# Optimization experiments

Measured on AMD Instinct MI355X. Metric: run time of the kernel, lower is better.

## Reference

```python
import jax, jax.numpy as jnp
import numpy as np

B, N, G = 16, 6000, 512
NUM_PAD_GT = 64  # zero-padded gt rows per image


def _make_boxes(key, shape):
    # sample two corner points and sort so (y1,x1) <= (y2,x2)
    r = jax.random.uniform(key, shape[:-1] + (4,), dtype=jnp.float32)
    lo = jnp.minimum(r[..., :2], r[..., 2:])
    hi = jnp.maximum(r[..., :2], r[..., 2:])
    return jnp.concatenate([lo, hi], axis=-1)


def setup_inputs() -> dict:
    key = jax.random.key(0)
    k1, k2, k3 = jax.random.split(key, 3)
    rois = _make_boxes(k1, (B, N, 4))
    gt_boxes = _make_boxes(k2, (B, G, 4))
    # zero-pad tail gt rows (remove_zero_padding signal)
    gt_boxes = gt_boxes.at[:, G - NUM_PAD_GT:, :].set(0.0)
    # ids in [-2, 18]: <0 crowd, ==0 padding, >0 real classes
    gt_ids = jax.random.randint(k3, (B, G), 0, 21, dtype=jnp.int64) - 2
    gt_ids = jnp.where(jnp.arange(G) >= G - NUM_PAD_GT, 0, gt_ids)
    return {"rois": rois, "gt_ids": gt_ids, "gt_boxes": gt_boxes}


def _pairwise_iou(boxes1, boxes2):
    # boxes1: [B,N,4], boxes2: [B,G,4] in (y1,x1,y2,x2) -> IoU [B,N,G]
    b1 = boxes1[:, :, None, :]  # [B,N,1,4]
    b2 = boxes2[:, None, :, :]  # [B,1,G,4]
    y1 = jnp.maximum(b1[..., 0], b2[..., 0])
    x1 = jnp.maximum(b1[..., 1], b2[..., 1])
    y2 = jnp.minimum(b1[..., 2], b2[..., 2])
    x2 = jnp.minimum(b1[..., 3], b2[..., 3])
    inter = jnp.maximum(y2 - y1, 0.0) * jnp.maximum(x2 - x1, 0.0)
    area1 = (b1[..., 2] - b1[..., 0]) * (b1[..., 3] - b1[..., 1])
    area2 = (b2[..., 2] - b2[..., 0]) * (b2[..., 3] - b2[..., 1])
    union = area1 + area2 - inter
    return inter / (union + 1e-8)


def reference(rois, gt_ids, gt_boxes):
    # remove_zero_padding -> validity masks (jit-friendly: mask instead of gather)
    valid_roi = jnp.sum(jnp.abs(rois), axis=-1) > 0.0      # [B,N]
    valid_gt = jnp.sum(jnp.abs(gt_boxes), axis=-1) > 0.0   # [B,G]
    crowd = valid_gt & (gt_ids < 0)                          # [B,G]
    non_crowd = valid_gt & (gt_ids > 0)                      # [B,G]

    iou = _pairwise_iou(rois, gt_boxes)                      # [B,N,G]
    # max IoU against non-crowd / crowd gt subsets (masked cols -> 0, IoU >= 0)
    iou_nc_max = jnp.max(jnp.where(non_crowd[:, None, :], iou, 0.0), axis=2)
    iou_c_max = jnp.max(jnp.where(crowd[:, None, :], iou, 0.0), axis=2)
    iou_nc_max = jnp.where(valid_roi, iou_nc_max, 0.0)       # [B,N]
    iou_c_max = jnp.where(valid_roi, iou_c_max, 0.0)

    positive_mask = valid_roi & (iou_nc_max >= 0.5)
    negative_mask = valid_roi & (iou_nc_max < 0.5) & (iou_c_max < 1e-3)

    iou_maxes = jnp.stack([iou_nc_max, iou_c_max], axis=1)   # [B,2,N]
    return iou_maxes, positive_mask, negative_mask
```

## Files before the change

kernel.cpp:

```cpp
#include <hip/hip_runtime.h>

#define BB 16
#define NN 6000
#define GG 512
#define WAVES 8
#define ROIS_PER_BLOCK 128

__global__ __launch_bounds__(64 * WAVES) void det_kernel(
    const float4* __restrict__ rois,
    const int*    __restrict__ gt_ids,
    const float4* __restrict__ gt_boxes,
    float*        __restrict__ out)
{
    __shared__ float4 s_box[GG];
    __shared__ float4 s_area4[GG / 4];
    __shared__ float  s_ncm[WAVES][ROIS_PER_BLOCK];
    __shared__ float  s_cm[WAVES][ROIS_PER_BLOCK];
    __shared__ int    s_cnt[2];
    __shared__ int    s_bounds[2];
    float* s_area = (float*)s_area4;

    const int b    = blockIdx.y;
    const int tid  = threadIdx.x;
    const int wave = tid >> 6;
    const int lane = tid & 63;

    if (tid == 0) { s_cnt[0] = 0; s_cnt[1] = 0; }
    __syncthreads();

    {
        const int g = tid;
        float4 box = gt_boxes[b * GG + g];
        float asum = fabsf(box.x) + fabsf(box.y) + fabsf(box.z) + fabsf(box.w);
        int id = gt_ids[b * GG + g];
        const bool pn = (asum > 0.0f) && (id > 0);
        const bool pc = (asum > 0.0f) && (id < 0);
        unsigned long long mn = __ballot(pn);
        unsigned long long mc = __ballot(pc);
        int bn = 0, bc = 0;
        if (lane == 0) {
            bn = atomicAdd(&s_cnt[0], __popcll(mn));
            bc = atomicAdd(&s_cnt[1], __popcll(mc));
        }
        bn = __shfl(bn, 0);
        bc = __shfl(bc, 0);
        const unsigned long long lt = (1ULL << lane) - 1ULL;
        if (pn) {
            int idx = bn + __popcll(mn & lt);
            s_box[idx]  = box;
            s_area[idx] = (box.z - box.x) * (box.w - box.y);
        }
        if (pc) {
            int idx = (GG - 1) - (bc + __popcll(mc & lt));
            s_box[idx]  = box;
            s_area[idx] = (box.z - box.x) * (box.w - box.y);
        }
    }
    __syncthreads();

    if (tid == 0) {
        int ncnt = s_cnt[0];
        int lo   = GG - s_cnt[1];
        int nc_eff = (ncnt + 3) & ~3;
        int lo_pad = lo & ~3;
        if (nc_eff > lo_pad) nc_eff = lo_pad;
        s_bounds[0] = nc_eff;
        s_bounds[1] = lo_pad;
    }
    __syncthreads();

    const int nc_eff = s_bounds[0];
    const int lo_pad = s_bounds[1];

    {
        const float4 z = make_float4(0.f, 0.f, 0.f, 0.f);
        const int ncnt = s_cnt[0];
        const int lo   = GG - s_cnt[1];
        if (tid < 4) {
            int i = ncnt + tid;
            if (i < nc_eff) { s_box[i] = z; s_area[i] = 0.f; }
        } else if (tid < 8) {
            int i = lo_pad + (tid - 4);
            if (i < lo) { s_box[i] = z; s_area[i] = 0.f; }
        }
    }
    __syncthreads();

    const int nbase = blockIdx.x * ROIS_PER_BLOCK;
    const int n0 = nbase + lane;
    const int n1 = nbase + 64 + lane;
    const float4 z4 = make_float4(0.f, 0.f, 0.f, 0.f);
    const float4 r0 = (n0 < NN) ? rois[b * NN + n0] : z4;
    const float4 r1 = (n1 < NN) ? rois[b * NN + n1] : z4;
    const bool  v0 = (fabsf(r0.x) + fabsf(r0.y) + fabsf(r0.z) + fabsf(r0.w)) > 0.0f;
    const bool  v1 = (fabsf(r1.x) + fabsf(r1.y) + fabsf(r1.z) + fabsf(r1.w)) > 0.0f;
    const float rs0 = (r0.z - r0.x) * (r0.w - r0.y) + 1e-8f;
    const float rs1 = (r1.z - r1.x) * (r1.w - r1.y) + 1e-8f;

    auto iou_of = [](const float4& rr, float rsum, const float4& g4, float ga) -> float {
        float yy1 = fmaxf(rr.x, g4.x);
        float xx1 = fmaxf(rr.y, g4.y);
        float yy2 = fminf(rr.z, g4.z);
        float xx2 = fminf(rr.w, g4.w);
        float inter = fmaxf(yy2 - yy1, 0.0f) * fmaxf(xx2 - xx1, 0.0f);
        float uni = rsum + ga - inter;
        return inter * __builtin_amdgcn_rcpf(uni);
    };

    float nc0 = 0.f, nc1 = 0.f, c0 = 0.f, c1 = 0.f;

    {
        const int ngr = nc_eff >> 2;
        const int gpw = (ngr + WAVES - 1) / WAVES;
        const int q0 = wave * gpw;
        const int q1 = min(ngr, q0 + gpw);
        for (int q = q0; q < q1; ++q) {
            float4 b0 = s_box[4 * q + 0];
            float4 b1 = s_box[4 * q + 1];
            float4 b2 = s_box[4 * q + 2];
            float4 b3 = s_box[4 * q + 3];
            float4 a4 = s_area4[q];
            nc0 = fmaxf(nc0, fmaxf(fmaxf(iou_of(r0, rs0, b0, a4.x), iou_of(r0, rs0, b1, a4.y)),
                                   fmaxf(iou_of(r0, rs0, b2, a4.z), iou_of(r0, rs0, b3, a4.w))));
            nc1 = fmaxf(nc1, fmaxf(fmaxf(iou_of(r1, rs1, b0, a4.x), iou_of(r1, rs1, b1, a4.y)),
                                   fmaxf(iou_of(r1, rs1, b2, a4.z), iou_of(r1, rs1, b3, a4.w))));
        }
    }
    {
        const int cg0 = lo_pad >> 2;
        const int cgn = (GG >> 2) - cg0;
        const int gpw = (cgn + WAVES - 1) / WAVES;
        const int q0 = cg0 + wave * gpw;
        const int q1 = min(GG >> 2, q0 + gpw);
        for (int q = q0; q < q1; ++q) {
            float4 b0 = s_box[4 * q + 0];
            float4 b1 = s_box[4 * q + 1];
            float4 b2 = s_box[4 * q + 2];
            float4 b3 = s_box[4 * q + 3];
            float4 a4 = s_area4[q];
            c0 = fmaxf(c0, fmaxf(fmaxf(iou_of(r0, rs0, b0, a4.x), iou_of(r0, rs0, b1, a4.y)),
                                 fmaxf(iou_of(r0, rs0, b2, a4.z), iou_of(r0, rs0, b3, a4.w))));
            c1 = fmaxf(c1, fmaxf(fmaxf(iou_of(r1, rs1, b0, a4.x), iou_of(r1, rs1, b1, a4.y)),
                                 fmaxf(iou_of(r1, rs1, b2, a4.z), iou_of(r1, rs1, b3, a4.w))));
        }
    }

    s_ncm[wave][lane]      = nc0;
    s_ncm[wave][64 + lane] = nc1;
    s_cm[wave][lane]       = c0;
    s_cm[wave][64 + lane]  = c1;
    __syncthreads();

    if (wave < 2) {
        const int i = wave * 64 + lane;
        const int n = nbase + i;
        if (n < NN) {
            const bool  vr = (wave == 0) ? v0 : v1;
            float a = s_ncm[0][i], c = s_cm[0][i];
            #pragma unroll
            for (int w = 1; w < WAVES; ++w) {
                a = fmaxf(a, s_ncm[w][i]);
                c = fmaxf(c, s_cm[w][i]);
            }
            const float nc_max = vr ? a : 0.0f;
            const float c_max  = vr ? c : 0.0f;

            out[b * 2 * NN + n]      = nc_max;
            out[b * 2 * NN + NN + n] = c_max;
            const float pos = (vr && nc_max >= 0.5f) ? 1.0f : 0.0f;
            const float neg = (vr && nc_max < 0.5f && c_max < 0.001f) ? 1.0f : 0.0f;
            out[BB * 2 * NN + b * NN + n]           = pos;
            out[BB * 2 * NN + BB * NN + b * NN + n] = neg;
        }
    }
}

extern "C" void kernel_launch(void* const* d_in, const int* in_sizes, int n_in,
                              void* d_out, int out_size, void* d_ws, size_t ws_size,
                              hipStream_t stream) {
    const float4* rois     = (const float4*)d_in[0];
    const int*    gt_ids   = (const int*)d_in[1];
    const float4* gt_boxes = (const float4*)d_in[2];
    float*        out      = (float*)d_out;

    dim3 grid((NN + ROIS_PER_BLOCK - 1) / ROIS_PER_BLOCK, BB);
    det_kernel<<<grid, 64 * WAVES, 0, stream>>>(rois, gt_ids, gt_boxes, out);
}
```

Baseline: 27.97 us.

## Max over inter/(sum of areas) and convert to IoU once; three ROIs per thread

Each thread now handles three ROIs instead of two, which spreads the reuse of every shared-memory GT box load over more work and shrinks the grid. The inner loop no longer computes union = sum - inter. It takes the max of t = inter/(area1+area2) and recovers IoU once per ROI as t/(1-t), which is monotonic in IoU. That removes a subtraction per pair but adds some rounding differences. The ROI validity flag is staged through shared memory, at the cost of more registers per thread and a less even last block.

```diff
diff --git a/kernel.cpp b/kernel.cpp
--- a/kernel.cpp
+++ b/kernel.cpp
@@ -4,7 +4,8 @@
 #define NN 6000
 #define GG 512
 #define WAVES 8
-#define ROIS_PER_BLOCK 128
+#define RPT 3
+#define RPB (RPT * 64)
 
 __global__ __launch_bounds__(64 * WAVES) void det_kernel(
     const float4* __restrict__ rois,
@@ -14,8 +15,9 @@
 {
     __shared__ float4 s_box[GG];
     __shared__ float4 s_area4[GG / 4];
-    __shared__ float  s_ncm[WAVES][ROIS_PER_BLOCK];
-    __shared__ float  s_cm[WAVES][ROIS_PER_BLOCK];
+    __shared__ float  s_ncm[WAVES][RPB];
+    __shared__ float  s_cm[WAVES][RPB];
+    __shared__ float  s_val[RPB];
     __shared__ int    s_cnt[2];
     __shared__ int    s_bounds[2];
     float* s_area = (float*)s_area4;
@@ -86,28 +88,29 @@
     }
     __syncthreads();
 
-    const int nbase = blockIdx.x * ROIS_PER_BLOCK;
-    const int n0 = nbase + lane;
-    const int n1 = nbase + 64 + lane;
-    const float4 z4 = make_float4(0.f, 0.f, 0.f, 0.f);
-    const float4 r0 = (n0 < NN) ? rois[b * NN + n0] : z4;
-    const float4 r1 = (n1 < NN) ? rois[b * NN + n1] : z4;
-    const bool  v0 = (fabsf(r0.x) + fabsf(r0.y) + fabsf(r0.z) + fabsf(r0.w)) > 0.0f;
-    const bool  v1 = (fabsf(r1.x) + fabsf(r1.y) + fabsf(r1.z) + fabsf(r1.w)) > 0.0f;
-    const float rs0 = (r0.z - r0.x) * (r0.w - r0.y) + 1e-8f;
-    const float rs1 = (r1.z - r1.x) * (r1.w - r1.y) + 1e-8f;
-
-    auto iou_of = [](const float4& rr, float rsum, const float4& g4, float ga) -> float {
-        float yy1 = fmaxf(rr.x, g4.x);
-        float xx1 = fmaxf(rr.y, g4.y);
-        float yy2 = fminf(rr.z, g4.z);
-        float xx2 = fminf(rr.w, g4.w);
-        float inter = fmaxf(yy2 - yy1, 0.0f) * fmaxf(xx2 - xx1, 0.0f);
-        float uni = rsum + ga - inter;
-        return inter * __builtin_amdgcn_rcpf(uni);
+    const int nbase = blockIdx.x * RPB;
+    float4 r[RPT];
+    float  rs[RPT];
+    #pragma unroll
+    for (int i = 0; i < RPT; ++i) {
+        int n = nbase + i * 64 + lane;
+        float4 rr = (n < NN) ? rois[b * NN + n] : make_float4(0.f, 0.f, 0.f, 0.f);
+        r[i]  = rr;
+        rs[i] = (rr.z - rr.x) * (rr.w - rr.y) + 1e-8f;
+        if (wave == 0)
+            s_val[i * 64 + lane] =
+                ((fabsf(rr.x) + fabsf(rr.y) + fabsf(rr.z) + fabsf(rr.w)) > 0.f) ? 1.f : 0.f;
+    }
+
+    auto tval = [](const float4& rr, float rsum, const float4& g4, float ga) -> float {
+        float dy = fminf(rr.z, g4.z) - fmaxf(rr.x, g4.x);
+        float dx = fminf(rr.w, g4.w) - fmaxf(rr.y, g4.y);
+        float inter = fmaxf(fmaxf(dy, 0.f) * dx, 0.f);
+        return inter * __builtin_amdgcn_rcpf(rsum + ga);
     };
 
-    float nc0 = 0.f, nc1 = 0.f, c0 = 0.f, c1 = 0.f;
+    float anc[RPT] = {0.f, 0.f, 0.f};
+    float ac[RPT]  = {0.f, 0.f, 0.f};
 
     {
         const int ngr = nc_eff >> 2;
@@ -120,10 +123,14 @@
             float4 b2 = s_box[4 * q + 2];
             float4 b3 = s_box[4 * q + 3];
             float4 a4 = s_area4[q];
-            nc0 = fmaxf(nc0, fmaxf(fmaxf(iou_of(r0, rs0, b0, a4.x), iou_of(r0, rs0, b1, a4.y)),
-                                   fmaxf(iou_of(r0, rs0, b2, a4.z), iou_of(r0, rs0, b3, a4.w))));
-            nc1 = fmaxf(nc1, fmaxf(fmaxf(iou_of(r1, rs1, b0, a4.x), iou_of(r1, rs1, b1, a4.y)),
-                                   fmaxf(iou_of(r1, rs1, b2, a4.z), iou_of(r1, rs1, b3, a4.w))));
+            #pragma unroll
+            for (int i = 0; i < RPT; ++i) {
+                float t0 = tval(r[i], rs[i], b0, a4.x);
+                float t1 = tval(r[i], rs[i], b1, a4.y);
+                float t2 = tval(r[i], rs[i], b2, a4.z);
+                float t3 = tval(r[i], rs[i], b3, a4.w);
+                anc[i] = fmaxf(anc[i], fmaxf(fmaxf(t0, t1), fmaxf(t2, t3)));
+            }
         }
     }
     {
@@ -138,37 +145,43 @@
             float4 b2 = s_box[4 * q + 2];
             float4 b3 = s_box[4 * q + 3];
             float4 a4 = s_area4[q];
-            c0 = fmaxf(c0, fmaxf(fmaxf(iou_of(r0, rs0, b0, a4.x), iou_of(r0, rs0, b1, a4.y)),
-                                 fmaxf(iou_of(r0, rs0, b2, a4.z), iou_of(r0, rs0, b3, a4.w))));
-            c1 = fmaxf(c1, fmaxf(fmaxf(iou_of(r1, rs1, b0, a4.x), iou_of(r1, rs1, b1, a4.y)),
-                                 fmaxf(iou_of(r1, rs1, b2, a4.z), iou_of(r1, rs1, b3, a4.w))));
-        }
-    }
-
-    s_ncm[wave][lane]      = nc0;
-    s_ncm[wave][64 + lane] = nc1;
-    s_cm[wave][lane]       = c0;
-    s_cm[wave][64 + lane]  = c1;
-    __syncthreads();
-
-    if (wave < 2) {
-        const int i = wave * 64 + lane;
-        const int n = nbase + i;
+            #pragma unroll
+            for (int i = 0; i < RPT; ++i) {
+                float t0 = tval(r[i], rs[i], b0, a4.x);
+                float t1 = tval(r[i], rs[i], b1, a4.y);
+                float t2 = tval(r[i], rs[i], b2, a4.z);
+                float t3 = tval(r[i], rs[i], b3, a4.w);
+                ac[i] = fmaxf(ac[i], fmaxf(fmaxf(t0, t1), fmaxf(t2, t3)));
+            }
+        }
+    }
+
+    #pragma unroll
+    for (int i = 0; i < RPT; ++i) {
+        s_ncm[wave][i * 64 + lane] = anc[i];
+        s_cm[wave][i * 64 + lane]  = ac[i];
+    }
+    __syncthreads();
+
+    if (tid < RPB) {
+        const int n = nbase + tid;
         if (n < NN) {
-            const bool  vr = (wave == 0) ? v0 : v1;
-            float a = s_ncm[0][i], c = s_cm[0][i];
+            float a = s_ncm[0][tid], c = s_cm[0][tid];
             #pragma unroll
             for (int w = 1; w < WAVES; ++w) {
-                a = fmaxf(a, s_ncm[w][i]);
-                c = fmaxf(c, s_cm[w][i]);
+                a = fmaxf(a, s_ncm[w][tid]);
+                c = fmaxf(c, s_cm[w][tid]);
             }
-            const float nc_max = vr ? a : 0.0f;
-            const float c_max  = vr ? c : 0.0f;
+            const float vr = s_val[tid];
+            a *= vr;
+            c *= vr;
+            const float nc_max = a * __builtin_amdgcn_rcpf(1.f - a);
+            const float c_max  = c * __builtin_amdgcn_rcpf(1.f - c);
 
             out[b * 2 * NN + n]      = nc_max;
             out[b * 2 * NN + NN + n] = c_max;
-            const float pos = (vr && nc_max >= 0.5f) ? 1.0f : 0.0f;
-            const float neg = (vr && nc_max < 0.5f && c_max < 0.001f) ? 1.0f : 0.0f;
+            const float pos = (vr > 0.f && nc_max >= 0.5f) ? 1.0f : 0.0f;
+            const float neg = (vr > 0.f && nc_max < 0.5f && c_max < 0.001f) ? 1.0f : 0.0f;
             out[BB * 2 * NN + b * NN + n]           = pos;
             out[BB * 2 * NN + BB * NN + b * NN + n] = neg;
         }
@@ -183,6 +196,6 @@
     const float4* gt_boxes = (const float4*)d_in[2];
     float*        out      = (float*)d_out;
 
-    dim3 grid((NN + ROIS_PER_BLOCK - 1) / ROIS_PER_BLOCK, BB);
+    dim3 grid((NN + RPB - 1) / RPB, BB);
     det_kernel<<<grid, 64 * WAVES, 0, stream>>>(rois, gt_ids, gt_boxes, out);
 }
```

Measured after the change: 26.07 us. 6.8% less time.
